# Kernel tuning notes

Hardware: AMD Instinct MI355X
Metric: run time of the kernel (lower is better)

Reference implementation:

```python
import jax, jax.numpy as jnp
import numpy as np

B = 128          # batch
T = 196          # total_patches per view (2 views -> 2*T tokens)
ENC = 1024       # encoder_embed_dim
DEC = 512        # decoder_embed_dim
V = 98           # num unmasked (visible) tokens per sample
M = 2 * T - V    # num masked tokens (294)


def setup_inputs() -> dict:
    key = jax.random.key(0)
    kx, kperm, kw, kmt, kpos, kview = jax.random.split(key, 6)
    x = jax.random.normal(kx, (B, V, ENC), jnp.float32)
    # masked_ids: unique ids per row in [0, 2T) — built from permutations
    perms = jax.vmap(jax.random.permutation, in_axes=(0, None))(
        jax.random.split(kperm, B), 2 * T)
    masked_ids = perms[:, :M].astype(jnp.int64)
    W = jax.random.normal(kw, (DEC, ENC), jnp.float32) * 0.02
    b = jnp.zeros((DEC,), jnp.float32)
    mask_token = jax.random.normal(kmt, (1, 1, DEC), jnp.float32)
    pos_embed = jax.random.normal(kpos, (1, 2 * T, DEC), jnp.float32)
    view_embed = jax.random.normal(kview, (2, DEC), jnp.float32)
    return {"x": x, "masked_ids": masked_ids, "W": W, "b": b,
            "mask_token": mask_token, "pos_embed": pos_embed,
            "view_embed": view_embed}


def reference(x, masked_ids, W, b, mask_token, pos_embed, view_embed):
    Bn = x.shape[0]
    # Linear: enc -> dec
    xp = jnp.einsum('bve,de->bvd', x, W) + b          # (B, V, DEC)
    # visible ids = sorted complement of masked_ids (vectorized, no batch loop)
    rows = jnp.arange(Bn)[:, None]
    vis_mask = jnp.ones((Bn, 2 * T), bool).at[rows, masked_ids].set(False)
    # stable argsort puts True(visible, ~mask=False) positions first, in order
    visible_ids = jnp.argsort(~vis_mask, axis=1)[:, :V]  # (B, V)
    # scatter projected visible tokens into mask-token placeholders
    base = jnp.broadcast_to(mask_token, (Bn, 2 * T, DEC))
    view = base.at[rows, visible_ids].set(xp)          # (B, 2T, DEC)
    # per-view embedding: first T tokens -> view 0, last T -> view 1
    ve = jnp.concatenate([
        jnp.broadcast_to(view_embed[0], (T, DEC)),
        jnp.broadcast_to(view_embed[1], (T, DEC))], axis=0)  # (2T, DEC)
    return view + pos_embed + ve[None, :, :]
```

## Files before the change

### kernel.cpp

```cpp
#include <hip/hip_runtime.h>

#define BATCH 128
#define VIS   98
#define TOK   196
#define TOK2  392
#define ENC   1024
#define DEC   512
#define MSK   294

typedef __bf16 bf16x8 __attribute__((ext_vector_type(8)));
typedef float  f32x4  __attribute__((ext_vector_type(4)));

__device__ __forceinline__ unsigned short f2bf(float f) {
    union { float f; unsigned u; } c; c.f = f;
    unsigned u = c.u;
    return (unsigned short)((u + 0x7fffu + ((u >> 16) & 1u)) >> 16);
}

__device__ __forceinline__ bf16x8 cvt8(f32x4 lo, f32x4 hi) {
    union { unsigned short u[8]; bf16x8 v; } r;
    r.u[0] = f2bf(lo[0]); r.u[1] = f2bf(lo[1]); r.u[2] = f2bf(lo[2]); r.u[3] = f2bf(lo[3]);
    r.u[4] = f2bf(hi[0]); r.u[5] = f2bf(hi[1]); r.u[6] = f2bf(hi[2]); r.u[7] = f2bf(hi[3]);
    return r.v;
}

__device__ __forceinline__ void g2lds16(const void* gptr, void* lptr) {
    __builtin_amdgcn_global_load_lds(
        (const __attribute__((address_space(1))) void*)gptr,
        (__attribute__((address_space(3))) void*)lptr, 16, 0, 0);
}

__global__ __launch_bounds__(256) void cvt_bf16(const float* __restrict__ src,
                                                unsigned short* __restrict__ dst,
                                                int n4) {
    int i = blockIdx.x * 256 + threadIdx.x;
    if (i >= n4) return;
    float4 f = ((const float4*)src)[i];
    ushort4 o;
    o.x = f2bf(f.x); o.y = f2bf(f.y); o.z = f2bf(f.z); o.w = f2bf(f.w);
    ((ushort4*)dst)[i] = o;
}

__global__ __launch_bounds__(512) void build_map(const int* __restrict__ mids,
                                                 int* __restrict__ visids,
                                                 unsigned char* __restrict__ flags) {
    int b = blockIdx.x;
    __shared__ unsigned char lf[TOK2];
    __shared__ int wtot[8];
    int tid = threadIdx.x;
    if (tid < TOK2) lf[tid] = 1;
    __syncthreads();
    if (tid < MSK) lf[mids[b * MSK + tid]] = 0;
    __syncthreads();
    int flag = (tid < TOK2) ? (int)lf[tid] : 0;
    unsigned long long bal = __ballot(flag != 0);
    int lane = tid & 63, wv = tid >> 6;
    int pre = __popcll(bal & ((1ull << lane) - 1ull));
    if (lane == 0) wtot[wv] = __popcll(bal);
    __syncthreads();
    int off = 0;
    for (int i = 0; i < wv; ++i) off += wtot[i];
    if (flag) visids[b * VIS + off + pre] = tid;
    if (tid < TOK2) flags[b * TOK2 + tid] = lf[tid];
}

__global__ __launch_bounds__(256) void fill_masked(const unsigned char* __restrict__ flags,
                                                   const float* __restrict__ mask_token,
                                                   const float* __restrict__ pos,
                                                   const float* __restrict__ ve,
                                                   float* __restrict__ out) {
    int b = blockIdx.y;
    int g = blockIdx.x * 256 + threadIdx.x;
    int t  = g >> 7;
    int d4 = g & 127;
    int tok = b * TOK2 + t;
    if (flags[tok]) return;
    float4 m = ((const float4*)mask_token)[d4];
    float4 p = ((const float4*)(pos + (size_t)t * DEC))[d4];
    float4 v = ((const float4*)(ve + (t >= TOK ? DEC : 0)))[d4];
    float4 r;
    r.x = m.x + p.x + v.x;
    r.y = m.y + p.y + v.y;
    r.z = m.z + p.z + v.z;
    r.w = m.w + p.w + v.w;
    ((float4*)(out + (size_t)tok * DEC))[d4] = r;
}

__global__ __launch_bounds__(256, 2) void gemm_scatter(
    const float* __restrict__ x,
    const unsigned short* __restrict__ wb,
    const float* __restrict__ bias,
    const float* __restrict__ pos,
    const float* __restrict__ ve,
    const int* __restrict__ vis,
    float* __restrict__ out) {
    __shared__ float          As[128 * 64];
    __shared__ unsigned short Bs[128 * 64];
    __shared__ int rowdst[128];
    __shared__ int rowt[128];

    int tid = threadIdx.x;
    int lane = tid & 63, w = tid >> 6;
    int l16 = lane & 15, q = lane >> 4;
    int wm = w & 1, wn = w >> 1;
    int m0 = blockIdx.y * 128, n0 = blockIdx.x * 128;

    if (tid < 128) {
        int gr = m0 + tid;
        int t = vis[gr];
        rowt[tid] = t;
        rowdst[tid] = (gr / VIS) * TOK2 + t;
    }

    int cA = (tid & 15) ^ ((tid >> 4) & 15);
    const float* gA = x + (size_t)(m0 + (tid >> 4)) * ENC + cA * 4;
    int cB = (tid & 7) ^ ((tid >> 3) & 7);
    const unsigned short* gB = wb + (size_t)(n0 + (tid >> 3)) * ENC + cB * 8;
    char* ldsA = (char*)As + tid * 16;
    char* ldsB = (char*)Bs + tid * 16;

    f32x4 acc[4][4];
    #pragma unroll
    for (int i = 0; i < 4; ++i)
        #pragma unroll
        for (int j = 0; j < 4; ++j)
            acc[i][j] = (f32x4){0.f, 0.f, 0.f, 0.f};

    for (int k0 = 0; k0 < ENC; k0 += 64) {
        __syncthreads();
        #pragma unroll
        for (int t = 0; t < 8; ++t)
            g2lds16(gA + (size_t)t * 16 * ENC + k0, ldsA + t * 4096);
        #pragma unroll
        for (int t = 0; t < 4; ++t)
            g2lds16(gB + (size_t)t * 32 * ENC + k0, ldsB + t * 4096);
        __syncthreads();

        #pragma unroll
        for (int u = 0; u < 2; ++u) {
            bf16x8 bfrag[4];
            #pragma unroll
            for (int j = 0; j < 4; ++j) {
                int nrow = wn * 64 + j * 16 + l16;
                int p = (u * 4 + q) ^ (l16 & 7);
                bfrag[j] = *(const bf16x8*)((const char*)Bs + nrow * 128 + p * 16);
            }
            #pragma unroll
            for (int i = 0; i < 4; ++i) {
                int mrow = wm * 64 + i * 16 + l16;
                int p0 = (u * 8 + 2 * q) ^ l16;
                int p1 = (u * 8 + 2 * q + 1) ^ l16;
                f32x4 lo = *(const f32x4*)((const char*)As + mrow * 256 + p0 * 16);
                f32x4 hi = *(const f32x4*)((const char*)As + mrow * 256 + p1 * 16);
                bf16x8 afrag = cvt8(lo, hi);
                #pragma unroll
                for (int j = 0; j < 4; ++j)
                    acc[i][j] = __builtin_amdgcn_mfma_f32_16x16x32_bf16(afrag, bfrag[j], acc[i][j], 0, 0, 0);
            }
        }
    }

    #pragma unroll
    for (int j = 0; j < 4; ++j) {
        int gcol = n0 + wn * 64 + j * 16 + l16;
        float bc = bias[gcol];
        float v0 = ve[gcol];
        float v1 = ve[DEC + gcol];
        #pragma unroll
        for (int i = 0; i < 4; ++i) {
            #pragma unroll
            for (int r = 0; r < 4; ++r) {
                int rl = wm * 64 + i * 16 + q * 4 + r;
                int t = rowt[rl];
                float val = acc[i][j][r] + bc + pos[(size_t)t * DEC + gcol]
                          + (t >= TOK ? v1 : v0);
                out[(size_t)rowdst[rl] * DEC + gcol] = val;
            }
        }
    }
}

extern "C" void kernel_launch(void* const* d_in, const int* in_sizes, int n_in,
                              void* d_out, int out_size, void* d_ws, size_t ws_size,
                              hipStream_t stream) {
    (void)in_sizes; (void)n_in; (void)out_size; (void)ws_size;
    const float* x    = (const float*)d_in[0];
    const int*   mids = (const int*)d_in[1];
    const float* W    = (const float*)d_in[2];
    const float* bias = (const float*)d_in[3];
    const float* mt   = (const float*)d_in[4];
    const float* pos  = (const float*)d_in[5];
    const float* ve   = (const float*)d_in[6];
    float* out = (float*)d_out;

    unsigned short* wbm = (unsigned short*)d_ws;
    int* visids = (int*)(wbm + (size_t)DEC * ENC);
    unsigned char* flags = (unsigned char*)(visids + BATCH * VIS);

    int n4w = DEC * ENC / 4;
    hipLaunchKernelGGL(cvt_bf16, dim3((n4w + 255) / 256), dim3(256), 0, stream, W, wbm, n4w);
    hipLaunchKernelGGL(build_map, dim3(BATCH), dim3(512), 0, stream, mids, visids, flags);
    hipLaunchKernelGGL(fill_masked, dim3(TOK2 * 128 / 256, BATCH), dim3(256), 0, stream,
                       flags, mt, pos, ve, out);
    hipLaunchKernelGGL(gemm_scatter, dim3(4, (BATCH * VIS) / 128), dim3(256), 0, stream,
                       x, wbm, bias, pos, ve, visids, out);
}
```

Baseline: 189.4 us.

## Pre-convert activations to bf16 and merge setup kernels into one launch

A single setup kernel now converts both x and W to bf16 and builds the visibility map, replacing the separate W-convert and map kernels. The GEMM then stages bf16 A tiles in shared memory instead of fp32, which halves A traffic and LDS size and removes the per-fragment fp32-to-bf16 conversion from the inner loop. Launch bounds rise to 4 waves per SIMD to use the freed LDS. The cost is an extra pass that reads the full fp32 x and writes a bf16 copy to workspace before the GEMM runs.

```diff
diff --git a/kernel.cpp b/kernel.cpp
--- a/kernel.cpp
+++ b/kernel.cpp
@@ -8,6 +8,9 @@
 #define DEC   512
 #define MSK   294
 
+#define NXB 6272
+#define NWB 256
+
 typedef __bf16 bf16x8 __attribute__((ext_vector_type(8)));
 typedef float  f32x4  __attribute__((ext_vector_type(4)));
 
@@ -17,37 +20,33 @@
     return (unsigned short)((u + 0x7fffu + ((u >> 16) & 1u)) >> 16);
 }
 
-__device__ __forceinline__ bf16x8 cvt8(f32x4 lo, f32x4 hi) {
-    union { unsigned short u[8]; bf16x8 v; } r;
-    r.u[0] = f2bf(lo[0]); r.u[1] = f2bf(lo[1]); r.u[2] = f2bf(lo[2]); r.u[3] = f2bf(lo[3]);
-    r.u[4] = f2bf(hi[0]); r.u[5] = f2bf(hi[1]); r.u[6] = f2bf(hi[2]); r.u[7] = f2bf(hi[3]);
-    return r.v;
-}
-
 __device__ __forceinline__ void g2lds16(const void* gptr, void* lptr) {
     __builtin_amdgcn_global_load_lds(
         (const __attribute__((address_space(1))) void*)gptr,
         (__attribute__((address_space(3))) void*)lptr, 16, 0, 0);
 }
 
-__global__ __launch_bounds__(256) void cvt_bf16(const float* __restrict__ src,
-                                                unsigned short* __restrict__ dst,
-                                                int n4) {
-    int i = blockIdx.x * 256 + threadIdx.x;
-    if (i >= n4) return;
-    float4 f = ((const float4*)src)[i];
-    ushort4 o;
-    o.x = f2bf(f.x); o.y = f2bf(f.y); o.z = f2bf(f.z); o.w = f2bf(f.w);
-    ((ushort4*)dst)[i] = o;
-}
-
-__global__ __launch_bounds__(512) void build_map(const int* __restrict__ mids,
-                                                 int* __restrict__ visids,
-                                                 unsigned char* __restrict__ flags) {
-    int b = blockIdx.x;
+__global__ __launch_bounds__(512) void setup(const float* __restrict__ x,
+                                             const float* __restrict__ W,
+                                             const int* __restrict__ mids,
+                                             unsigned short* __restrict__ xb,
+                                             unsigned short* __restrict__ wbm,
+                                             int* __restrict__ visids,
+                                             unsigned char* __restrict__ flags) {
+    int bid = blockIdx.x, tid = threadIdx.x;
+    if (bid < NXB + NWB) {
+        const float* src = (bid < NXB) ? x : W;
+        unsigned short* dst = (bid < NXB) ? xb : wbm;
+        int i = (bid < NXB ? bid : bid - NXB) * 512 + tid;
+        float4 f = ((const float4*)src)[i];
+        ushort4 o;
+        o.x = f2bf(f.x); o.y = f2bf(f.y); o.z = f2bf(f.z); o.w = f2bf(f.w);
+        ((ushort4*)dst)[i] = o;
+        return;
+    }
+    int b = bid - NXB - NWB;
     __shared__ unsigned char lf[TOK2];
     __shared__ int wtot[8];
-    int tid = threadIdx.x;
     if (tid < TOK2) lf[tid] = 1;
     __syncthreads();
     if (tid < MSK) lf[mids[b * MSK + tid]] = 0;
@@ -86,15 +85,15 @@
     ((float4*)(out + (size_t)tok * DEC))[d4] = r;
 }
 
-__global__ __launch_bounds__(256, 2) void gemm_scatter(
-    const float* __restrict__ x,
+__global__ __launch_bounds__(256, 4) void gemm_scatter(
+    const unsigned short* __restrict__ xb,
     const unsigned short* __restrict__ wb,
     const float* __restrict__ bias,
     const float* __restrict__ pos,
     const float* __restrict__ ve,
     const int* __restrict__ vis,
     float* __restrict__ out) {
-    __shared__ float          As[128 * 64];
+    __shared__ unsigned short As[128 * 64];
     __shared__ unsigned short Bs[128 * 64];
     __shared__ int rowdst[128];
     __shared__ int rowt[128];
@@ -112,10 +111,9 @@
         rowdst[tid] = (gr / VIS) * TOK2 + t;
     }
 
-    int cA = (tid & 15) ^ ((tid >> 4) & 15);
-    const float* gA = x + (size_t)(m0 + (tid >> 4)) * ENC + cA * 4;
-    int cB = (tid & 7) ^ ((tid >> 3) & 7);
-    const unsigned short* gB = wb + (size_t)(n0 + (tid >> 3)) * ENC + cB * 8;
+    int c = (tid & 7) ^ ((tid >> 3) & 7);
+    const unsigned short* gA = xb + (size_t)(m0 + (tid >> 3)) * ENC + c * 8;
+    const unsigned short* gB = wb + (size_t)(n0 + (tid >> 3)) * ENC + c * 8;
     char* ldsA = (char*)As + tid * 16;
     char* ldsB = (char*)Bs + tid * 16;
 
@@ -129,8 +127,8 @@
     for (int k0 = 0; k0 < ENC; k0 += 64) {
         __syncthreads();
         #pragma unroll
-        for (int t = 0; t < 8; ++t)
-            g2lds16(gA + (size_t)t * 16 * ENC + k0, ldsA + t * 4096);
+        for (int t = 0; t < 4; ++t)
+            g2lds16(gA + (size_t)t * 32 * ENC + k0, ldsA + t * 4096);
         #pragma unroll
         for (int t = 0; t < 4; ++t)
             g2lds16(gB + (size_t)t * 32 * ENC + k0, ldsB + t * 4096);
@@ -138,25 +136,19 @@
 
         #pragma unroll
         for (int u = 0; u < 2; ++u) {
-            bf16x8 bfrag[4];
+            int slot = ((u * 4 + q) ^ (l16 & 7)) * 16;
+            bf16x8 bfrag[4], afrag[4];
             #pragma unroll
-            for (int j = 0; j < 4; ++j) {
-                int nrow = wn * 64 + j * 16 + l16;
-                int p = (u * 4 + q) ^ (l16 & 7);
-                bfrag[j] = *(const bf16x8*)((const char*)Bs + nrow * 128 + p * 16);
-            }
+            for (int j = 0; j < 4; ++j)
+                bfrag[j] = *(const bf16x8*)((const char*)Bs + (wn * 64 + j * 16 + l16) * 128 + slot);
             #pragma unroll
-            for (int i = 0; i < 4; ++i) {
-                int mrow = wm * 64 + i * 16 + l16;
-                int p0 = (u * 8 + 2 * q) ^ l16;
-                int p1 = (u * 8 + 2 * q + 1) ^ l16;
-                f32x4 lo = *(const f32x4*)((const char*)As + mrow * 256 + p0 * 16);
-                f32x4 hi = *(const f32x4*)((const char*)As + mrow * 256 + p1 * 16);
-                bf16x8 afrag = cvt8(lo, hi);
+            for (int i = 0; i < 4; ++i)
+                afrag[i] = *(const bf16x8*)((const char*)As + (wm * 64 + i * 16 + l16) * 128 + slot);
+            #pragma unroll
+            for (int i = 0; i < 4; ++i)
                 #pragma unroll
                 for (int j = 0; j < 4; ++j)
-                    acc[i][j] = __builtin_amdgcn_mfma_f32_16x16x32_bf16(afrag, bfrag[j], acc[i][j], 0, 0, 0);
-            }
+                    acc[i][j] = __builtin_amdgcn_mfma_f32_16x16x32_bf16(afrag[i], bfrag[j], acc[i][j], 0, 0, 0);
         }
     }
 
@@ -193,15 +185,15 @@
     const float* ve   = (const float*)d_in[6];
     float* out = (float*)d_out;
 
-    unsigned short* wbm = (unsigned short*)d_ws;
+    unsigned short* xb = (unsigned short*)d_ws;
+    unsigned short* wbm = xb + (size_t)BATCH * VIS * ENC;
     int* visids = (int*)(wbm + (size_t)DEC * ENC);
     unsigned char* flags = (unsigned char*)(visids + BATCH * VIS);
 
-    int n4w = DEC * ENC / 4;
-    hipLaunchKernelGGL(cvt_bf16, dim3((n4w + 255) / 256), dim3(256), 0, stream, W, wbm, n4w);
-    hipLaunchKernelGGL(build_map, dim3(BATCH), dim3(512), 0, stream, mids, visids, flags);
+    hipLaunchKernelGGL(setup, dim3(NXB + NWB + BATCH), dim3(512), 0, stream,
+                       x, W, mids, xb, wbm, visids, flags);
     hipLaunchKernelGGL(fill_masked, dim3(TOK2 * 128 / 256, BATCH), dim3(256), 0, stream,
                        flags, mt, pos, ve, out);
     hipLaunchKernelGGL(gemm_scatter, dim3(4, (BATCH * VIS) / 128), dim3(256), 0, stream,
-                       x, wbm, bias, pos, ve, visids, out);
+                       xb, wbm, bias, pos, ve, visids, out);
 }
```

Measured after the change: 191.2 us. About the same (+0.9%).
